# Kernel optimization log

Measured on AMD Instinct MI355X. Metric: run time of the kernel, lower is better.

## Reference

```python
import jax, jax.numpy as jnp
import numpy as np

NEG_SLOPE = 0.2
EPS = 1e-16

def gatv2(x, edge_index, edge_attr, Wl, bl, We, att, bias):
    """PyG GATv2Conv, heads=1, share_weights=True, with edge_dim."""
    N = x.shape[0]
    h = x @ Wl + bl                      # [N, out] shared lin_l == lin_r
    src, dst = edge_index[0], edge_index[1]
    hj = h[src]                          # source (message) features [E, out]
    hi = h[dst]                          # target features [E, out]
    e = jax.nn.leaky_relu(hi + hj + edge_attr @ We, NEG_SLOPE)  # [E, out]
    score = e @ att                      # [E]
    # segment softmax over edges grouped by destination node
    smax = jax.ops.segment_max(score, dst, num_segments=N)
    ex = jnp.exp(score - smax[dst])
    denom = jax.ops.segment_sum(ex, dst, num_segments=N)
    alpha = ex / (denom[dst] + EPS)      # [E]
    out = jax.ops.segment_sum(hj * alpha[:, None], dst, num_segments=N)
    return out + bias


def setup_inputs() -> dict:
    key = jax.random.key(0)
    N, E = 50000, 800000
    D_IN, D_LAT, D_EDGE, N_ACT = 128, 128, 16, 32
    ks = jax.random.split(key, 16)
    s = 0.05
    inp = {
        "x": jax.random.normal(ks[0], (N, D_IN), jnp.float32),
        "edge_index": jax.random.randint(ks[1], (2, E), 0, N, jnp.int32),
        "edge_attr": jax.random.normal(ks[2], (E, D_EDGE), jnp.float32),
        # gnn_layer: D_IN -> D_LAT
        "Wl1": jax.random.normal(ks[3], (D_IN, D_LAT), jnp.float32) * s,
        "bl1": jnp.zeros((D_LAT,), jnp.float32),
        "We1": jax.random.normal(ks[4], (D_EDGE, D_LAT), jnp.float32) * s,
        "att1": jax.random.normal(ks[5], (D_LAT,), jnp.float32) * s,
        "bias1": jnp.zeros((D_LAT,), jnp.float32),
        # node_layer: D_LAT -> 1
        "Wl2": jax.random.normal(ks[6], (D_LAT, 1), jnp.float32) * s,
        "bl2": jnp.zeros((1,), jnp.float32),
        "We2": jax.random.normal(ks[7], (D_EDGE, 1), jnp.float32) * s,
        "att2": jax.random.normal(ks[8], (1,), jnp.float32) * s,
        "bias2": jnp.zeros((1,), jnp.float32),
        # action_layer: D_LAT -> N_ACT
        "Wl3": jax.random.normal(ks[9], (D_LAT, N_ACT), jnp.float32) * s,
        "bl3": jnp.zeros((N_ACT,), jnp.float32),
        "We3": jax.random.normal(ks[10], (D_EDGE, N_ACT), jnp.float32) * s,
        "att3": jax.random.normal(ks[11], (N_ACT,), jnp.float32) * s,
        "bias3": jnp.zeros((N_ACT,), jnp.float32),
    }
    return inp


def reference(x, edge_index, edge_attr,
              Wl1, bl1, We1, att1, bias1,
              Wl2, bl2, We2, att2, bias2,
              Wl3, bl3, We3, att3, bias3):
    latent = gatv2(x, edge_index, edge_attr, Wl1, bl1, We1, att1, bias1)          # [N, D_LAT]
    node_logits = gatv2(latent, edge_index, edge_attr, Wl2, bl2, We2, att2, bias2)[:, 0]  # [N]
    action_logits = gatv2(latent, edge_index, edge_attr, Wl3, bl3, We3, att3, bias3)      # [N, A]
    # categorical sampling with fixed key (deterministic reference)
    k1, k2 = jax.random.split(jax.random.key(42))
    node_sel = jax.random.categorical(k1, node_logits)
    node_lp = jax.nn.log_softmax(node_logits)[node_sel]
    act_logits_sel = action_logits[node_sel, :]
    action_sel = jax.random.categorical(k2, act_logits_sel)
    action_lp = jax.nn.log_softmax(act_logits_sel)[action_sel]
    return (node_sel, action_sel, node_lp + action_lp)
```

## Files before the change

### kernel.cpp

```cpp
#include <hip/hip_runtime.h>
#include <stdint.h>
#include <math.h>

#define NEG 0.2f
#define TINYF 1.1754943508222875e-38f

__host__ __device__ inline void threefry2x32(uint32_t k0, uint32_t k1,
                                             uint32_t x0, uint32_t x1,
                                             uint32_t* o0, uint32_t* o1) {
  uint32_t ks0 = k0, ks1 = k1, ks2 = k0 ^ k1 ^ 0x1BD11BDAu;
  x0 += ks0; x1 += ks1;
#define RR(r) { x0 += x1; x1 = (x1 << (r)) | (x1 >> (32 - (r))); x1 ^= x0; }
  RR(13) RR(15) RR(26) RR(6)
  x0 += ks1; x1 += ks2 + 1u;
  RR(17) RR(29) RR(16) RR(24)
  x0 += ks2; x1 += ks0 + 2u;
  RR(13) RR(15) RR(26) RR(6)
  x0 += ks0; x1 += ks1 + 3u;
  RR(17) RR(29) RR(16) RR(24)
  x0 += ks1; x1 += ks2 + 4u;
  RR(13) RR(15) RR(26) RR(6)
  x0 += ks2; x1 += ks0 + 5u;
#undef RR
  *o0 = x0; *o1 = x1;
}

__device__ inline float gumbel_part(uint32_t ka, uint32_t kb, uint32_t i) {
  uint32_t o0, o1;
  threefry2x32(ka, kb, 0u, i, &o0, &o1);
  uint32_t bits = o0 ^ o1;
  float f = __uint_as_float((bits >> 9) | 0x3f800000u) - 1.0f;
  float u = fmaxf(TINYF, f + TINYF);
  return -logf(-logf(u));
}

__global__ void count_kernel(const int* __restrict__ ei, int E, int* __restrict__ counts) {
  int e = blockIdx.x * blockDim.x + threadIdx.x;
  if (e < E) atomicAdd(&counts[ei[E + e]], 1);
}

__global__ __launch_bounds__(1024) void scan_kernel(const int* __restrict__ counts,
    int* __restrict__ row_start, int* __restrict__ cursor, int N, int E) {
  __shared__ int wsum[16];
  __shared__ int base_s;
  int tid = threadIdx.x;
  int lane = tid & 63, wv = tid >> 6;
  if (tid == 0) base_s = 0;
  __syncthreads();
  for (int chunk = 0; chunk < N; chunk += 1024) {
    int i = chunk + tid;
    int v = (i < N) ? counts[i] : 0;
    int incl = v;
#pragma unroll
    for (int off = 1; off < 64; off <<= 1) {
      int t = __shfl_up(incl, off);
      if (lane >= off) incl += t;
    }
    if (lane == 63) wsum[wv] = incl;
    __syncthreads();
    if (wv == 0) {
      int x = (lane < 16) ? wsum[lane] : 0;
#pragma unroll
      for (int off = 1; off < 16; off <<= 1) {
        int t = __shfl_up(x, off);
        if (lane >= off) x += t;
      }
      if (lane < 16) wsum[lane] = x;
    }
    __syncthreads();
    int waveoff = (wv == 0) ? 0 : wsum[wv - 1];
    int base = base_s;
    int excl = base + waveoff + incl - v;
    if (i < N) { row_start[i] = excl; cursor[i] = excl; }
    __syncthreads();
    if (tid == 1023) base_s = base + wsum[15];
    __syncthreads();
  }
  if (tid == 0) row_start[N] = base_s;
}

__global__ void scatter_kernel(const int* __restrict__ ei, const float* __restrict__ ea,
                               int E, int* __restrict__ cursor,
                               int* __restrict__ src_csr, float* __restrict__ ea_csr) {
  int e = blockIdx.x * blockDim.x + threadIdx.x;
  if (e < E) {
    int d = ei[E + e];
    int p = atomicAdd(&cursor[d], 1);
    src_csr[p] = ei[e];
    const float4* s4 = (const float4*)&ea[(size_t)e * 16];
    float4* d4 = (float4*)&ea_csr[(size_t)p * 16];
    float4 t0 = s4[0], t1 = s4[1], t2 = s4[2], t3 = s4[3];
    d4[0] = t0; d4[1] = t1; d4[2] = t2; d4[3] = t3;
  }
}

__global__ __launch_bounds__(256) void gemm128_kernel(const float* __restrict__ X,
    const float* __restrict__ W, const float* __restrict__ bias,
    float* __restrict__ out, int M) {
  __shared__ float xs[128][33];
  int row0 = blockIdx.x * 32;
  int tid = threadIdx.x;
  for (int idx = tid; idx < 32 * 128; idx += 256) {
    int r = idx >> 7;
    int k = idx & 127;
    int row = row0 + r;
    xs[k][r] = (row < M) ? X[(size_t)row * 128 + k] : 0.0f;
  }
  __syncthreads();
  int tc = tid & 31, tr = tid >> 5;
  int c0 = tc * 4, r0 = tr * 4;
  float acc[4][4] = {};
#pragma unroll 4
  for (int k = 0; k < 128; k++) {
    float4 w = *(const float4*)&W[k * 128 + c0];
    float x0 = xs[k][r0], x1 = xs[k][r0 + 1], x2 = xs[k][r0 + 2], x3 = xs[k][r0 + 3];
    acc[0][0] += x0 * w.x; acc[0][1] += x0 * w.y; acc[0][2] += x0 * w.z; acc[0][3] += x0 * w.w;
    acc[1][0] += x1 * w.x; acc[1][1] += x1 * w.y; acc[1][2] += x1 * w.z; acc[1][3] += x1 * w.w;
    acc[2][0] += x2 * w.x; acc[2][1] += x2 * w.y; acc[2][2] += x2 * w.z; acc[2][3] += x2 * w.w;
    acc[3][0] += x3 * w.x; acc[3][1] += x3 * w.y; acc[3][2] += x3 * w.z; acc[3][3] += x3 * w.w;
  }
  float4 b4 = *(const float4*)&bias[c0];
  for (int r = 0; r < 4; r++) {
    int row = row0 + r0 + r;
    if (row < M) {
      float4 o;
      o.x = acc[r][0] + b4.x; o.y = acc[r][1] + b4.y;
      o.z = acc[r][2] + b4.z; o.w = acc[r][3] + b4.w;
      *(float4*)&out[(size_t)row * 128 + c0] = o;
    }
  }
}

__global__ __launch_bounds__(256) void gemm32_kernel(const float* __restrict__ X,
    const float* __restrict__ W, const float* __restrict__ bias,
    float* __restrict__ out, int M) {
  int t = blockIdx.x * 256 + threadIdx.x;
  int node = t >> 5, c = t & 31;
  if (node >= M) return;
  const float4* xp = (const float4*)&X[(size_t)node * 128];
  float acc = 0.f;
#pragma unroll
  for (int q = 0; q < 32; q++) {
    float4 x4 = xp[q];
    acc += x4.x * W[(q * 4 + 0) * 32 + c] + x4.y * W[(q * 4 + 1) * 32 + c]
         + x4.z * W[(q * 4 + 2) * 32 + c] + x4.w * W[(q * 4 + 3) * 32 + c];
  }
  out[(size_t)node * 32 + c] = acc + bias[c];
}

__global__ __launch_bounds__(256) void gemv_kernel(const float* __restrict__ X,
    const float* __restrict__ w, const float* __restrict__ b0,
    float* __restrict__ out, int M) {
  int wv = (blockIdx.x * 256 + threadIdx.x) >> 6;
  int lane = threadIdx.x & 63;
  if (wv >= M) return;
  float2 xv = *(const float2*)&X[(size_t)wv * 128 + lane * 2];
  float2 wvv = *(const float2*)&w[lane * 2];
  float v = xv.x * wvv.x + xv.y * wvv.y;
#pragma unroll
  for (int off = 32; off; off >>= 1) v += __shfl_xor(v, off);
  if (lane == 0) out[wv] = v + b0[0];
}

__global__ __launch_bounds__(256) void fused1_kernel(const float* __restrict__ h,
    const int* __restrict__ src_csr, const int* __restrict__ row_start,
    const float* __restrict__ ea_csr,
    const float* __restrict__ We, const float* __restrict__ att,
    const float* __restrict__ bias, float* __restrict__ out, int N) {
  __shared__ float WeS[2048];
  int tid = threadIdx.x;
  for (int i = tid; i < 2048; i += 256) WeS[i] = We[i];
  __syncthreads();
  int hw = (blockIdx.x * 256 + tid) >> 5;
  int lane = tid & 31;
  if (hw >= N) return;
  int c4 = lane * 4;
  float4 attv = *(const float4*)&att[c4];
  float4 b4 = *(const float4*)&bias[c4];
  int start = row_start[hw];
  int deg = row_start[hw + 1] - start;
  if (deg == 0) {
    *(float4*)&out[(size_t)hw * 128 + c4] = b4;
    return;
  }
  float4 hi = *(const float4*)&h[(size_t)hw * 128 + c4];
  int s_l = (lane < deg) ? src_csr[start + lane] : 0;
  int dcap = deg < 32 ? deg : 32;
  const float4* eap = (const float4*)&ea_csr[(size_t)start * 16];
  float m = -INFINITY, l = 0.f;
  float4 acc = make_float4(0.f, 0.f, 0.f, 0.f);
  for (int j = 0; j < deg; j++) {
    int s = (j < dcap) ? __shfl(s_l, j, 32) : src_csr[start + j];
    float4 hj = *(const float4*)&h[(size_t)s * 128 + c4];
    float4 v;
    v.x = hi.x + hj.x; v.y = hi.y + hj.y; v.z = hi.z + hj.z; v.w = hi.w + hj.w;
#pragma unroll
    for (int q = 0; q < 4; q++) {
      float4 aq = eap[(size_t)j * 4 + q];
      float4 w0 = *(const float4*)&WeS[(4 * q + 0) * 128 + c4];
      float4 w1 = *(const float4*)&WeS[(4 * q + 1) * 128 + c4];
      float4 w2 = *(const float4*)&WeS[(4 * q + 2) * 128 + c4];
      float4 w3 = *(const float4*)&WeS[(4 * q + 3) * 128 + c4];
      v.x += aq.x * w0.x + aq.y * w1.x + aq.z * w2.x + aq.w * w3.x;
      v.y += aq.x * w0.y + aq.y * w1.y + aq.z * w2.y + aq.w * w3.y;
      v.z += aq.x * w0.z + aq.y * w1.z + aq.z * w2.z + aq.w * w3.z;
      v.w += aq.x * w0.w + aq.y * w1.w + aq.z * w2.w + aq.w * w3.w;
    }
    v.x = v.x >= 0.f ? v.x : NEG * v.x;
    v.y = v.y >= 0.f ? v.y : NEG * v.y;
    v.z = v.z >= 0.f ? v.z : NEG * v.z;
    v.w = v.w >= 0.f ? v.w : NEG * v.w;
    float sc = v.x * attv.x + v.y * attv.y + v.z * attv.z + v.w * attv.w;
#pragma unroll
    for (int off = 16; off; off >>= 1) sc += __shfl_xor(sc, off);
    float mn = fmaxf(m, sc);
    float scale = __expf(m - mn);
    float w = __expf(sc - mn);
    l = l * scale + w;
    acc.x = acc.x * scale + w * hj.x;
    acc.y = acc.y * scale + w * hj.y;
    acc.z = acc.z * scale + w * hj.z;
    acc.w = acc.w * scale + w * hj.w;
    m = mn;
  }
  float inv = 1.0f / (l + 1e-16f);
  float4 o;
  o.x = acc.x * inv + b4.x;
  o.y = acc.y * inv + b4.y;
  o.z = acc.z * inv + b4.z;
  o.w = acc.w * inv + b4.w;
  *(float4*)&out[(size_t)hw * 128 + c4] = o;
}

__global__ __launch_bounds__(256) void fused23_kernel(
    const float* __restrict__ h3, const float* __restrict__ h2,
    const int* __restrict__ src_csr, const int* __restrict__ row_start,
    const float* __restrict__ ea_csr,
    const float* __restrict__ We3, const float* __restrict__ att3,
    const float* __restrict__ bias3, const float* __restrict__ We2,
    const float* __restrict__ att2, const float* __restrict__ bias2,
    float* __restrict__ out3, float* __restrict__ logits, int N) {
  int tid = threadIdx.x;
  int wv = (blockIdx.x * 256 + tid) >> 6;
  int lane = tid & 63;
  if (wv >= N) return;
  int q4 = lane >> 4;
  int l16 = lane & 15;
  int c2 = l16 * 2;
  float2 we3[16];
#pragma unroll
  for (int k = 0; k < 16; k++) we3[k] = *(const float2*)&We3[k * 32 + c2];
  float we2[16];
#pragma unroll
  for (int k = 0; k < 16; k++) we2[k] = We2[k];
  float2 at3 = *(const float2*)&att3[c2];
  float a2s = att2[0];
  float2 bi3 = *(const float2*)&bias3[c2];
  int start = row_start[wv];
  int deg = row_start[wv + 1] - start;
  if (deg == 0) {
    if (lane < 16) *(float2*)&out3[(size_t)wv * 32 + c2] = bi3;
    if (lane == 0) logits[wv] = bias2[0];
    return;
  }
  float2 hi3 = *(const float2*)&h3[(size_t)wv * 32 + c2];
  float hi2 = h2[wv];
  int s_l = (lane < deg) ? src_csr[start + lane] : 0;
  int dcap = deg < 64 ? deg : 64;
  const float4* eap = (const float4*)&ea_csr[(size_t)start * 16];
  float m3 = -INFINITY, l3 = 0.f; float2 a3 = make_float2(0.f, 0.f);
  float m2 = -INFINITY, l2 = 0.f; float a2 = 0.f;
  for (int j = q4; j < deg; j += 4) {
    int s = (j < dcap) ? __shfl(s_l, j) : src_csr[start + j];
    float2 hj3 = *(const float2*)&h3[(size_t)s * 32 + c2];
    float h2s = h2[s];
    float4 c0 = eap[(size_t)j * 4 + 0];
    float4 c1 = eap[(size_t)j * 4 + 1];
    float4 cc2 = eap[(size_t)j * 4 + 2];
    float4 c3 = eap[(size_t)j * 4 + 3];
    float vx = hi3.x + hj3.x, vy = hi3.y + hj3.y;
    vx += c0.x * we3[0].x + c0.y * we3[1].x + c0.z * we3[2].x + c0.w * we3[3].x;
    vy += c0.x * we3[0].y + c0.y * we3[1].y + c0.z * we3[2].y + c0.w * we3[3].y;
    vx += c1.x * we3[4].x + c1.y * we3[5].x + c1.z * we3[6].x + c1.w * we3[7].x;
    vy += c1.x * we3[4].y + c1.y * we3[5].y + c1.z * we3[6].y + c1.w * we3[7].y;
    vx += cc2.x * we3[8].x + cc2.y * we3[9].x + cc2.z * we3[10].x + cc2.w * we3[11].x;
    vy += cc2.x * we3[8].y + cc2.y * we3[9].y + cc2.z * we3[10].y + cc2.w * we3[11].y;
    vx += c3.x * we3[12].x + c3.y * we3[13].x + c3.z * we3[14].x + c3.w * we3[15].x;
    vy += c3.x * we3[12].y + c3.y * we3[13].y + c3.z * we3[14].y + c3.w * we3[15].y;
    vx = vx >= 0.f ? vx : NEG * vx;
    vy = vy >= 0.f ? vy : NEG * vy;
    float t3 = vx * at3.x + vy * at3.y;
#pragma unroll
    for (int off = 8; off; off >>= 1) t3 += __shfl_xor(t3, off);
    float v2 = hi2 + h2s;
    v2 += c0.x * we2[0]  + c0.y * we2[1]  + c0.z * we2[2]  + c0.w * we2[3];
    v2 += c1.x * we2[4]  + c1.y * we2[5]  + c1.z * we2[6]  + c1.w * we2[7];
    v2 += cc2.x * we2[8] + cc2.y * we2[9] + cc2.z * we2[10] + cc2.w * we2[11];
    v2 += c3.x * we2[12] + c3.y * we2[13] + c3.z * we2[14] + c3.w * we2[15];
    v2 = v2 >= 0.f ? v2 : NEG * v2;
    float t2 = v2 * a2s;
    float mn3 = fmaxf(m3, t3);
    float sc3 = __expf(m3 - mn3);
    float w3 = __expf(t3 - mn3);
    l3 = l3 * sc3 + w3;
    a3.x = a3.x * sc3 + w3 * hj3.x;
    a3.y = a3.y * sc3 + w3 * hj3.y;
    m3 = mn3;
    float mn2 = fmaxf(m2, t2);
    float sc2 = __expf(m2 - mn2);
    float w2 = __expf(t2 - mn2);
    l2 = l2 * sc2 + w2;
    a2 = a2 * sc2 + w2 * h2s;
    m2 = mn2;
  }
#pragma unroll
  for (int off = 16; off <= 32; off <<= 1) {
    float m3o = __shfl_xor(m3, off), l3o = __shfl_xor(l3, off);
    float ax = __shfl_xor(a3.x, off), ay = __shfl_xor(a3.y, off);
    float M3 = fmaxf(m3, m3o);
    float sA = (m3 == -INFINITY) ? 0.f : __expf(m3 - M3);
    float sB = (m3o == -INFINITY) ? 0.f : __expf(m3o - M3);
    l3 = l3 * sA + l3o * sB;
    a3.x = a3.x * sA + ax * sB;
    a3.y = a3.y * sA + ay * sB;
    m3 = M3;
    float m2o = __shfl_xor(m2, off), l2o = __shfl_xor(l2, off);
    float az = __shfl_xor(a2, off);
    float M2 = fmaxf(m2, m2o);
    float tA = (m2 == -INFINITY) ? 0.f : __expf(m2 - M2);
    float tB = (m2o == -INFINITY) ? 0.f : __expf(m2o - M2);
    l2 = l2 * tA + l2o * tB;
    a2 = a2 * tA + az * tB;
    m2 = M2;
  }
  if (lane < 16) {
    float2 o;
    o.x = a3.x / (l3 + 1e-16f) + bi3.x;
    o.y = a3.y / (l3 + 1e-16f) + bi3.y;
    *(float2*)&out3[(size_t)wv * 32 + c2] = o;
  }
  if (lane == 0) logits[wv] = a2 / (l2 + 1e-16f) + bias2[0];
}

#define NSB 64
__global__ __launch_bounds__(256) void node_partial_kernel(const float* __restrict__ logits,
    int N, uint32_t ka, uint32_t kb,
    float* __restrict__ pB, int* __restrict__ pI,
    float* __restrict__ pM, float* __restrict__ pL) {
  int chunk = (N + NSB - 1) / NSB;
  int s0 = blockIdx.x * chunk;
  int s1 = s0 + chunk; if (s1 > N) s1 = N;
  int tid = threadIdx.x;
  float best = -INFINITY; int bi = 0x7fffffff;
  float m = -INFINITY, l = 0.f;
  for (int i = s0 + tid; i < s1; i += 256) {
    float lg = logits[i];
    float mn = fmaxf(m, lg);
    l = l * __expf(m - mn) + __expf(lg - mn);
    m = mn;
    float v = lg + gumbel_part(ka, kb, (uint32_t)i);
    if (v > best) { best = v; bi = i; }
  }
  __shared__ float sb[256], sm[256], sl[256];
  __shared__ int si[256];
  sb[tid] = best; si[tid] = bi; sm[tid] = m; sl[tid] = l;
  __syncthreads();
  for (int s = 128; s; s >>= 1) {
    if (tid < s) {
      if (sb[tid + s] > sb[tid] || (sb[tid + s] == sb[tid] && si[tid + s] < si[tid])) {
        sb[tid] = sb[tid + s]; si[tid] = si[tid + s];
      }
      float M = fmaxf(sm[tid], sm[tid + s]);
      float t0 = (sm[tid] == -INFINITY) ? 0.f : sl[tid] * __expf(sm[tid] - M);
      float t1 = (sm[tid + s] == -INFINITY) ? 0.f : sl[tid + s] * __expf(sm[tid + s] - M);
      sm[tid] = M; sl[tid] = t0 + t1;
    }
    __syncthreads();
  }
  if (tid == 0) { pB[blockIdx.x] = sb[0]; pI[blockIdx.x] = si[0]; pM[blockIdx.x] = sm[0]; pL[blockIdx.x] = sl[0]; }
}

__global__ __launch_bounds__(64) void node_final_kernel(const float* __restrict__ logits,
    const float* __restrict__ pB, const int* __restrict__ pI,
    const float* __restrict__ pM, const float* __restrict__ pL,
    float* __restrict__ scal) {
  int lane = threadIdx.x;
  float best = pB[lane]; int bi = pI[lane];
  float m = pM[lane]; float l = pL[lane];
#pragma unroll
  for (int off = 32; off; off >>= 1) {
    float ob = __shfl_xor(best, off); int oi = __shfl_xor(bi, off);
    if (ob > best || (ob == best && oi < bi)) { best = ob; bi = oi; }
    float om = __shfl_xor(m, off); float ol = __shfl_xor(l, off);
    float M = fmaxf(m, om);
    float t0 = (m == -INFINITY) ? 0.f : l * __expf(m - M);
    float t1 = (om == -INFINITY) ? 0.f : ol * __expf(om - M);
    m = M; l = t0 + t1;
  }
  if (lane == 0) {
    ((int*)scal)[0] = bi;
    scal[3] = logits[bi] - (m + logf(l));
  }
}

__global__ __launch_bounds__(64) void action_kernel(const float* __restrict__ out3,
    const float* __restrict__ scal, uint32_t ka, uint32_t kb,
    float* __restrict__ dout, int out_size) {
  int lane = threadIdx.x;
  int sel = ((const int*)scal)[0];
  float v = -INFINITY, noisy = -INFINITY;
  if (lane < 32) {
    v = out3[(size_t)sel * 32 + lane];
    noisy = v + gumbel_part(ka, kb, (uint32_t)lane);
  }
  int idx = lane;
  float nv = noisy;
#pragma unroll
  for (int off = 32; off; off >>= 1) {
    float ov = __shfl_xor(nv, off);
    int oi = __shfl_xor(idx, off);
    if (ov > nv || (ov == nv && oi < idx)) { nv = ov; idx = oi; }
  }
  float vm = v;
#pragma unroll
  for (int off = 32; off; off >>= 1) vm = fmaxf(vm, __shfl_xor(vm, off));
  float ex = (lane < 32) ? expf(v - vm) : 0.f;
#pragma unroll
  for (int off = 32; off; off >>= 1) ex += __shfl_xor(ex, off);
  float vsel = __shfl(v, idx);
  if (lane == 0) {
    float action_lp = vsel - vm - logf(ex);
    dout[0] = (float)sel;
    dout[1] = (float)idx;
    dout[2] = scal[3] + action_lp;
  }
  for (int i = 3 + lane; i < out_size; i += 64) dout[i] = 0.f;
}

extern "C" void kernel_launch(void* const* d_in, const int* in_sizes, int n_in,
                              void* d_out, int out_size, void* d_ws, size_t ws_size,
                              hipStream_t stream) {
  const float* x     = (const float*)d_in[0];
  const int*   ei    = (const int*)d_in[1];
  const float* ea    = (const float*)d_in[2];
  const float* Wl1   = (const float*)d_in[3];
  const float* bl1   = (const float*)d_in[4];
  const float* We1   = (const float*)d_in[5];
  const float* att1  = (const float*)d_in[6];
  const float* bias1 = (const float*)d_in[7];
  const float* Wl2   = (const float*)d_in[8];
  const float* bl2   = (const float*)d_in[9];
  const float* We2   = (const float*)d_in[10];
  const float* att2  = (const float*)d_in[11];
  const float* bias2 = (const float*)d_in[12];
  const float* Wl3   = (const float*)d_in[13];
  const float* bl3   = (const float*)d_in[14];
  const float* We3   = (const float*)d_in[15];
  const float* att3  = (const float*)d_in[16];
  const float* bias3 = (const float*)d_in[17];
  int N = in_sizes[0] / 128;
  int E = in_sizes[1] / 2;
  float* out = (float*)d_out;

  char* p = (char*)d_ws;
  auto alloc = [&](size_t bytes) -> char* {
    char* r = p; p += (bytes + 255) & ~(size_t)255; return r;
  };
  float* h1      = (float*)alloc((size_t)N * 128 * 4);
  float* latent  = (float*)alloc((size_t)N * 128 * 4);
  float* h3      = (float*)alloc((size_t)N * 32 * 4);
  float* h2      = (float*)alloc((size_t)N * 4);
  float* logits  = (float*)alloc((size_t)N * 4);
  float* out3    = (float*)alloc((size_t)N * 32 * 4);
  int* counts    = (int*)alloc((size_t)N * 4);
  int* row_start = (int*)alloc((size_t)(N + 1) * 4);
  int* cursor    = (int*)alloc((size_t)N * 4);
  int* src_csr   = (int*)alloc((size_t)E * 4);
  float* ea_csr  = (float*)alloc((size_t)E * 16 * 4);
  float* pB      = (float*)alloc(NSB * 4);
  int*   pI      = (int*)alloc(NSB * 4);
  float* pM      = (float*)alloc(NSB * 4);
  float* pL      = (float*)alloc(NSB * 4);
  float* scal    = (float*)alloc(64);
  (void)ws_size; (void)n_in;

  uint32_t k1a, k1b, k2a, k2b;
  threefry2x32(0u, 42u, 0u, 0u, &k1a, &k1b);
  threefry2x32(0u, 42u, 0u, 1u, &k2a, &k2b);

  hipMemsetAsync(counts, 0, (size_t)N * 4, stream);
  count_kernel<<<(E + 255) / 256, 256, 0, stream>>>(ei, E, counts);
  scan_kernel<<<1, 1024, 0, stream>>>(counts, row_start, cursor, N, E);
  scatter_kernel<<<(E + 255) / 256, 256, 0, stream>>>(ei, ea, E, cursor, src_csr, ea_csr);

  gemm128_kernel<<<(N + 31) / 32, 256, 0, stream>>>(x, Wl1, bl1, h1, N);
  fused1_kernel<<<(N + 7) / 8, 256, 0, stream>>>(h1, src_csr, row_start,
                                                 ea_csr, We1, att1, bias1, latent, N);

  gemm32_kernel<<<((size_t)N * 32 + 255) / 256, 256, 0, stream>>>(latent, Wl3, bl3, h3, N);
  gemv_kernel<<<(N + 3) / 4, 256, 0, stream>>>(latent, Wl2, bl2, h2, N);

  fused23_kernel<<<(N + 3) / 4, 256, 0, stream>>>(h3, h2, src_csr, row_start, ea_csr,
                                                  We3, att3, bias3, We2, att2, bias2,
                                                  out3, logits, N);

  node_partial_kernel<<<NSB, 256, 0, stream>>>(logits, N, k1a, k1b, pB, pI, pM, pL);
  node_final_kernel<<<1, 64, 0, stream>>>(logits, pB, pI, pM, pL, scal);
  action_kernel<<<1, 64, 0, stream>>>(out3, scal, k2a, k2b, out, out_size);
}
```

Measured before the change: 626.2 us.

## Parallelize CSR prefix scan across blocks and stage edge weights in LDS

The single-block serial scan over all node counts becomes a three-kernel multi-block scan: per-block partial sums, a single-block offset scan, then a per-block apply. fused1 is rewritten with clang ext_vector types so the edge-feature projection compiles to packed vector FMAs. fused23 loads We3, att3 and We2 into shared memory instead of holding them in per-thread registers, which should lower register pressure and raise occupancy. The scan now costs two extra kernel launches, and fused23 gains a block barrier plus extra LDS reads inside the edge loop.

```diff
diff --git a/kernel.cpp b/kernel.cpp
--- a/kernel.cpp
+++ b/kernel.cpp
@@ -4,6 +4,9 @@
 
 #define NEG 0.2f
 #define TINYF 1.1754943508222875e-38f
+
+typedef float f4 __attribute__((ext_vector_type(4)));
+typedef float f2 __attribute__((ext_vector_type(2)));
 
 __host__ __device__ inline void threefry2x32(uint32_t k0, uint32_t k1,
                                              uint32_t x0, uint32_t x1,
@@ -39,17 +42,56 @@
   if (e < E) atomicAdd(&counts[ei[E + e]], 1);
 }
 
-__global__ __launch_bounds__(1024) void scan_kernel(const int* __restrict__ counts,
-    int* __restrict__ row_start, int* __restrict__ cursor, int N, int E) {
-  __shared__ int wsum[16];
+#define SCB 256
+__global__ __launch_bounds__(256) void scan_partial_kernel(const int* __restrict__ counts,
+    int N, int chunk, int* __restrict__ bsum) {
+  int b = blockIdx.x;
+  int s0 = b * chunk, s1 = s0 + chunk; if (s1 > N) s1 = N;
+  int tid = threadIdx.x;
+  int v = 0;
+  for (int i = s0 + tid; i < s1; i += 256) v += counts[i];
+  __shared__ int red[256];
+  red[tid] = v; __syncthreads();
+  for (int s = 128; s; s >>= 1) { if (tid < s) red[tid] += red[tid + s]; __syncthreads(); }
+  if (tid == 0) bsum[b] = red[0];
+}
+
+__global__ __launch_bounds__(256) void scan_offsets_kernel(const int* __restrict__ bsum,
+    int* __restrict__ boff, int* __restrict__ row_start, int N) {
+  int tid = threadIdx.x; int lane = tid & 63; int wv = tid >> 6;
+  __shared__ int wsum[4];
+  int v = bsum[tid];
+  int incl = v;
+#pragma unroll
+  for (int off = 1; off < 64; off <<= 1) {
+    int t = __shfl_up(incl, off);
+    if (lane >= off) incl += t;
+  }
+  if (lane == 63) wsum[wv] = incl;
+  __syncthreads();
+  if (tid == 0) {
+    int s = 0;
+    for (int k = 0; k < 4; k++) { int t = wsum[k]; wsum[k] = s; s += t; }
+    row_start[N] = s;
+  }
+  __syncthreads();
+  boff[tid] = wsum[wv] + incl - v;
+}
+
+__global__ __launch_bounds__(256) void scan_apply_kernel(const int* __restrict__ counts,
+    const int* __restrict__ boff, int N, int chunk,
+    int* __restrict__ row_start, int* __restrict__ cursor) {
+  int b = blockIdx.x;
+  int s0 = b * chunk, s1 = s0 + chunk; if (s1 > N) s1 = N;
+  int tid = threadIdx.x; int lane = tid & 63; int wv = tid >> 6;
+  __shared__ int wsum[4];
+  __shared__ int tot_s;
   __shared__ int base_s;
-  int tid = threadIdx.x;
-  int lane = tid & 63, wv = tid >> 6;
-  if (tid == 0) base_s = 0;
-  __syncthreads();
-  for (int chunk = 0; chunk < N; chunk += 1024) {
-    int i = chunk + tid;
-    int v = (i < N) ? counts[i] : 0;
+  if (tid == 0) base_s = boff[b];
+  __syncthreads();
+  for (int c0 = s0; c0 < s1; c0 += 256) {
+    int i = c0 + tid;
+    int v = (i < s1) ? counts[i] : 0;
     int incl = v;
 #pragma unroll
     for (int off = 1; off < 64; off <<= 1) {
@@ -58,25 +100,19 @@
     }
     if (lane == 63) wsum[wv] = incl;
     __syncthreads();
-    if (wv == 0) {
-      int x = (lane < 16) ? wsum[lane] : 0;
-#pragma unroll
-      for (int off = 1; off < 16; off <<= 1) {
-        int t = __shfl_up(x, off);
-        if (lane >= off) x += t;
-      }
-      if (lane < 16) wsum[lane] = x;
+    if (tid == 0) {
+      int s = 0;
+      for (int k = 0; k < 4; k++) { int t = wsum[k]; wsum[k] = s; s += t; }
+      tot_s = s;
     }
     __syncthreads();
-    int waveoff = (wv == 0) ? 0 : wsum[wv - 1];
     int base = base_s;
-    int excl = base + waveoff + incl - v;
-    if (i < N) { row_start[i] = excl; cursor[i] = excl; }
+    int excl = base + wsum[wv] + incl - v;
+    if (i < s1) { row_start[i] = excl; cursor[i] = excl; }
     __syncthreads();
-    if (tid == 1023) base_s = base + wsum[15];
+    if (tid == 0) base_s = base + tot_s;
     __syncthreads();
   }
-  if (tid == 0) row_start[N] = base_s;
 }
 
 __global__ void scatter_kernel(const int* __restrict__ ei, const float* __restrict__ ea,
@@ -175,61 +211,51 @@
   int lane = tid & 31;
   if (hw >= N) return;
   int c4 = lane * 4;
-  float4 attv = *(const float4*)&att[c4];
-  float4 b4 = *(const float4*)&bias[c4];
+  const f4* W4 = (const f4*)WeS;
+  f4 attv = *(const f4*)&att[c4];
+  f4 bb = *(const f4*)&bias[c4];
   int start = row_start[hw];
   int deg = row_start[hw + 1] - start;
   if (deg == 0) {
-    *(float4*)&out[(size_t)hw * 128 + c4] = b4;
+    *(f4*)&out[(size_t)hw * 128 + c4] = bb;
     return;
   }
-  float4 hi = *(const float4*)&h[(size_t)hw * 128 + c4];
+  f4 hi = *(const f4*)&h[(size_t)hw * 128 + c4];
   int s_l = (lane < deg) ? src_csr[start + lane] : 0;
   int dcap = deg < 32 ? deg : 32;
-  const float4* eap = (const float4*)&ea_csr[(size_t)start * 16];
+  const f4* eap = (const f4*)&ea_csr[(size_t)start * 16];
   float m = -INFINITY, l = 0.f;
-  float4 acc = make_float4(0.f, 0.f, 0.f, 0.f);
+  f4 acc = (f4)0.f;
   for (int j = 0; j < deg; j++) {
     int s = (j < dcap) ? __shfl(s_l, j, 32) : src_csr[start + j];
-    float4 hj = *(const float4*)&h[(size_t)s * 128 + c4];
-    float4 v;
-    v.x = hi.x + hj.x; v.y = hi.y + hj.y; v.z = hi.z + hj.z; v.w = hi.w + hj.w;
+    f4 hj = *(const f4*)&h[(size_t)s * 128 + c4];
+    f4 v = hi + hj;
 #pragma unroll
     for (int q = 0; q < 4; q++) {
-      float4 aq = eap[(size_t)j * 4 + q];
-      float4 w0 = *(const float4*)&WeS[(4 * q + 0) * 128 + c4];
-      float4 w1 = *(const float4*)&WeS[(4 * q + 1) * 128 + c4];
-      float4 w2 = *(const float4*)&WeS[(4 * q + 2) * 128 + c4];
-      float4 w3 = *(const float4*)&WeS[(4 * q + 3) * 128 + c4];
-      v.x += aq.x * w0.x + aq.y * w1.x + aq.z * w2.x + aq.w * w3.x;
-      v.y += aq.x * w0.y + aq.y * w1.y + aq.z * w2.y + aq.w * w3.y;
-      v.z += aq.x * w0.z + aq.y * w1.z + aq.z * w2.z + aq.w * w3.z;
-      v.w += aq.x * w0.w + aq.y * w1.w + aq.z * w2.w + aq.w * w3.w;
+      f4 aq = eap[(size_t)j * 4 + q];
+      v += aq.x * W4[(4 * q + 0) * 32 + lane];
+      v += aq.y * W4[(4 * q + 1) * 32 + lane];
+      v += aq.z * W4[(4 * q + 2) * 32 + lane];
+      v += aq.w * W4[(4 * q + 3) * 32 + lane];
     }
     v.x = v.x >= 0.f ? v.x : NEG * v.x;
     v.y = v.y >= 0.f ? v.y : NEG * v.y;
     v.z = v.z >= 0.f ? v.z : NEG * v.z;
     v.w = v.w >= 0.f ? v.w : NEG * v.w;
-    float sc = v.x * attv.x + v.y * attv.y + v.z * attv.z + v.w * attv.w;
+    f4 pv = v * attv;
+    float sc = (pv.x + pv.y) + (pv.z + pv.w);
 #pragma unroll
     for (int off = 16; off; off >>= 1) sc += __shfl_xor(sc, off);
     float mn = fmaxf(m, sc);
     float scale = __expf(m - mn);
     float w = __expf(sc - mn);
     l = l * scale + w;
-    acc.x = acc.x * scale + w * hj.x;
-    acc.y = acc.y * scale + w * hj.y;
-    acc.z = acc.z * scale + w * hj.z;
-    acc.w = acc.w * scale + w * hj.w;
+    acc = acc * scale + w * hj;
     m = mn;
   }
   float inv = 1.0f / (l + 1e-16f);
-  float4 o;
-  o.x = acc.x * inv + b4.x;
-  o.y = acc.y * inv + b4.y;
-  o.z = acc.z * inv + b4.z;
-  o.w = acc.w * inv + b4.w;
-  *(float4*)&out[(size_t)hw * 128 + c4] = o;
+  f4 o = acc * inv + bb;
+  *(f4*)&out[(size_t)hw * 128 + c4] = o;
 }
 
 __global__ __launch_bounds__(256) void fused23_kernel(
@@ -240,71 +266,72 @@
     const float* __restrict__ bias3, const float* __restrict__ We2,
     const float* __restrict__ att2, const float* __restrict__ bias2,
     float* __restrict__ out3, float* __restrict__ logits, int N) {
+  __shared__ float We3S[512];
+  __shared__ float att3S[32];
+  __shared__ float We2S[16];
   int tid = threadIdx.x;
+  for (int i = tid; i < 512; i += 256) We3S[i] = We3[i];
+  if (tid < 32) att3S[tid] = att3[tid];
+  if (tid < 16) We2S[tid] = We2[tid];
+  __syncthreads();
   int wv = (blockIdx.x * 256 + tid) >> 6;
   int lane = tid & 63;
   if (wv >= N) return;
   int q4 = lane >> 4;
   int l16 = lane & 15;
   int c2 = l16 * 2;
-  float2 we3[16];
-#pragma unroll
-  for (int k = 0; k < 16; k++) we3[k] = *(const float2*)&We3[k * 32 + c2];
-  float we2[16];
-#pragma unroll
-  for (int k = 0; k < 16; k++) we2[k] = We2[k];
-  float2 at3 = *(const float2*)&att3[c2];
+  const f2* W3 = (const f2*)We3S;
+  f2 at3 = *(const f2*)&att3S[c2];
   float a2s = att2[0];
-  float2 bi3 = *(const float2*)&bias3[c2];
+  f2 bi3 = *(const f2*)&bias3[c2];
   int start = row_start[wv];
   int deg = row_start[wv + 1] - start;
   if (deg == 0) {
-    if (lane < 16) *(float2*)&out3[(size_t)wv * 32 + c2] = bi3;
+    if (lane < 16) *(f2*)&out3[(size_t)wv * 32 + c2] = bi3;
     if (lane == 0) logits[wv] = bias2[0];
     return;
   }
-  float2 hi3 = *(const float2*)&h3[(size_t)wv * 32 + c2];
+  f2 hi3 = *(const f2*)&h3[(size_t)wv * 32 + c2];
   float hi2 = h2[wv];
   int s_l = (lane < deg) ? src_csr[start + lane] : 0;
   int dcap = deg < 64 ? deg : 64;
   const float4* eap = (const float4*)&ea_csr[(size_t)start * 16];
-  float m3 = -INFINITY, l3 = 0.f; float2 a3 = make_float2(0.f, 0.f);
+  float m3 = -INFINITY, l3 = 0.f; f2 a3 = (f2)0.f;
   float m2 = -INFINITY, l2 = 0.f; float a2 = 0.f;
   for (int j = q4; j < deg; j += 4) {
     int s = (j < dcap) ? __shfl(s_l, j) : src_csr[start + j];
-    float2 hj3 = *(const float2*)&h3[(size_t)s * 32 + c2];
+    f2 hj3 = *(const f2*)&h3[(size_t)s * 32 + c2];
     float h2s = h2[s];
     float4 c0 = eap[(size_t)j * 4 + 0];
     float4 c1 = eap[(size_t)j * 4 + 1];
     float4 cc2 = eap[(size_t)j * 4 + 2];
     float4 c3 = eap[(size_t)j * 4 + 3];
-    float vx = hi3.x + hj3.x, vy = hi3.y + hj3.y;
-    vx += c0.x * we3[0].x + c0.y * we3[1].x + c0.z * we3[2].x + c0.w * we3[3].x;
-    vy += c0.x * we3[0].y + c0.y * we3[1].y + c0.z * we3[2].y + c0.w * we3[3].y;
-    vx += c1.x * we3[4].x + c1.y * we3[5].x + c1.z * we3[6].x + c1.w * we3[7].x;
-    vy += c1.x * we3[4].y + c1.y * we3[5].y + c1.z * we3[6].y + c1.w * we3[7].y;
-    vx += cc2.x * we3[8].x + cc2.y * we3[9].x + cc2.z * we3[10].x + cc2.w * we3[11].x;
-    vy += cc2.x * we3[8].y + cc2.y * we3[9].y + cc2.z * we3[10].y + cc2.w * we3[11].y;
-    vx += c3.x * we3[12].x + c3.y * we3[13].x + c3.z * we3[14].x + c3.w * we3[15].x;
-    vy += c3.x * we3[12].y + c3.y * we3[13].y + c3.z * we3[14].y + c3.w * we3[15].y;
-    vx = vx >= 0.f ? vx : NEG * vx;
-    vy = vy >= 0.f ? vy : NEG * vy;
-    float t3 = vx * at3.x + vy * at3.y;
+    f2 v = hi3 + hj3;
+    v += c0.x * W3[0 * 16 + l16];  v += c0.y * W3[1 * 16 + l16];
+    v += c0.z * W3[2 * 16 + l16];  v += c0.w * W3[3 * 16 + l16];
+    v += c1.x * W3[4 * 16 + l16];  v += c1.y * W3[5 * 16 + l16];
+    v += c1.z * W3[6 * 16 + l16];  v += c1.w * W3[7 * 16 + l16];
+    v += cc2.x * W3[8 * 16 + l16]; v += cc2.y * W3[9 * 16 + l16];
+    v += cc2.z * W3[10 * 16 + l16]; v += cc2.w * W3[11 * 16 + l16];
+    v += c3.x * W3[12 * 16 + l16]; v += c3.y * W3[13 * 16 + l16];
+    v += c3.z * W3[14 * 16 + l16]; v += c3.w * W3[15 * 16 + l16];
+    v.x = v.x >= 0.f ? v.x : NEG * v.x;
+    v.y = v.y >= 0.f ? v.y : NEG * v.y;
+    float t3 = v.x * at3.x + v.y * at3.y;
 #pragma unroll
     for (int off = 8; off; off >>= 1) t3 += __shfl_xor(t3, off);
     float v2 = hi2 + h2s;
-    v2 += c0.x * we2[0]  + c0.y * we2[1]  + c0.z * we2[2]  + c0.w * we2[3];
-    v2 += c1.x * we2[4]  + c1.y * we2[5]  + c1.z * we2[6]  + c1.w * we2[7];
-    v2 += cc2.x * we2[8] + cc2.y * we2[9] + cc2.z * we2[10] + cc2.w * we2[11];
-    v2 += c3.x * we2[12] + c3.y * we2[13] + c3.z * we2[14] + c3.w * we2[15];
+    v2 += c0.x * We2S[0]  + c0.y * We2S[1]  + c0.z * We2S[2]  + c0.w * We2S[3];
+    v2 += c1.x * We2S[4]  + c1.y * We2S[5]  + c1.z * We2S[6]  + c1.w * We2S[7];
+    v2 += cc2.x * We2S[8] + cc2.y * We2S[9] + cc2.z * We2S[10] + cc2.w * We2S[11];
+    v2 += c3.x * We2S[12] + c3.y * We2S[13] + c3.z * We2S[14] + c3.w * We2S[15];
     v2 = v2 >= 0.f ? v2 : NEG * v2;
     float t2 = v2 * a2s;
     float mn3 = fmaxf(m3, t3);
     float sc3 = __expf(m3 - mn3);
     float w3 = __expf(t3 - mn3);
     l3 = l3 * sc3 + w3;
-    a3.x = a3.x * sc3 + w3 * hj3.x;
-    a3.y = a3.y * sc3 + w3 * hj3.y;
+    a3 = a3 * sc3 + w3 * hj3;
     m3 = mn3;
     float mn2 = fmaxf(m2, t2);
     float sc2 = __expf(m2 - mn2);
@@ -334,10 +361,10 @@
     m2 = M2;
   }
   if (lane < 16) {
-    float2 o;
+    f2 o;
     o.x = a3.x / (l3 + 1e-16f) + bi3.x;
     o.y = a3.y / (l3 + 1e-16f) + bi3.y;
-    *(float2*)&out3[(size_t)wv * 32 + c2] = o;
+    *(f2*)&out3[(size_t)wv * 32 + c2] = o;
   }
   if (lane == 0) logits[wv] = a2 / (l2 + 1e-16f) + bias2[0];
 }
@@ -477,6 +504,8 @@
   int* cursor    = (int*)alloc((size_t)N * 4);
   int* src_csr   = (int*)alloc((size_t)E * 4);
   float* ea_csr  = (float*)alloc((size_t)E * 16 * 4);
+  int* bsum      = (int*)alloc(SCB * 4);
+  int* boff      = (int*)alloc(SCB * 4);
   float* pB      = (float*)alloc(NSB * 4);
   int*   pI      = (int*)alloc(NSB * 4);
   float* pM      = (float*)alloc(NSB * 4);
@@ -488,9 +517,13 @@
   threefry2x32(0u, 42u, 0u, 0u, &k1a, &k1b);
   threefry2x32(0u, 42u, 0u, 1u, &k2a, &k2b);
 
+  int chunk = (N + SCB - 1) / SCB;
+
   hipMemsetAsync(counts, 0, (size_t)N * 4, stream);
   count_kernel<<<(E + 255) / 256, 256, 0, stream>>>(ei, E, counts);
-  scan_kernel<<<1, 1024, 0, stream>>>(counts, row_start, cursor, N, E);
+  scan_partial_kernel<<<SCB, 256, 0, stream>>>(counts, N, chunk, bsum);
+  scan_offsets_kernel<<<1, 256, 0, stream>>>(bsum, boff, row_start, N);
+  scan_apply_kernel<<<SCB, 256, 0, stream>>>(counts, boff, N, chunk, row_start, cursor);
   scatter_kernel<<<(E + 255) / 256, 256, 0, stream>>>(ei, ea, E, cursor, src_csr, ea_csr);
 
   gemm128_kernel<<<(N + 31) / 32, 256, 0, stream>>>(x, Wl1, bl1, h1, N);
```

Result: faster. 584.6 us (-6.6%).
